# Kernel tuning notes

Hardware: AMD Instinct MI355X
Metric: run time of the kernel (lower is better)

Reference implementation:

```python
import jax, jax.numpy as jnp
import numpy as np

GAMMA = 2.0
EPS = 1e-6

B, C = 4096, 32000


def setup_inputs() -> dict:
    key = jax.random.key(0)
    k1, k2 = jax.random.split(key)
    pred = jax.random.normal(k1, (B, C), dtype=jnp.float32)
    target = jax.random.randint(k2, (B,), 0, C, dtype=jnp.int64)
    return {"pred": pred, "target": target}


def reference(pred, target):
    # pred: [B, C] logits, target: [B] int class labels
    b, c = pred.shape
    beta = (b - 1) / b
    logp = jax.nn.log_softmax(pred, axis=1)                      # [B, C]
    # Faithful to original: entropy_b = target_b * sum_c (1-p)^gamma * logp
    # (the torch code multiplies by the scalar class index b_target)
    focal = jnp.sum(jnp.power(1.0 - jnp.exp(logp), GAMMA) * logp, axis=1)  # [B]
    ent = target.astype(pred.dtype) * focal                     # [B]
    # class-balanced aggregation: bucket per class label
    counts = jax.ops.segment_sum(jnp.ones((b,), pred.dtype), target, num_segments=c)  # n_c
    cls_sum = jax.ops.segment_sum(ent, target, num_segments=c)  # sum of entropies per class
    w = (1.0 - beta) / (1.0 - jnp.power(jnp.asarray(beta, pred.dtype), counts) + EPS)
    # classes absent from batch have cls_sum == 0 exactly, so they contribute 0
    return (-1.0 / b) * jnp.sum(w * cls_sum)
```

## Files before the change

kernel.cpp:

```cpp
#include <hip/hip_runtime.h>
#include <math.h>

#define NROWS 4096
#define NCLS  32000
#define VEC_PER_ROW (NCLS / 4)
#define BLK 512
#define NV  16
#define TAIL (VEC_PER_ROW - (NV - 1) * BLK)
#define EPSF 1e-6f

#define LNBETA (-2.4417042724800387e-4f)
#define WNUM 2.44140625e-4f

__device__ __forceinline__ float max4(float4 v) {
    return fmaxf(fmaxf(v.x, v.y), fmaxf(v.z, v.w));
}
__device__ __forceinline__ float sum4(float4 v) {
    return (v.x + v.y) + (v.z + v.w);
}

__global__ __launch_bounds__(BLK, 4) void focal_kernel(const float* __restrict__ pred,
                                                       float* __restrict__ focal_out)
{
    const int row = blockIdx.x;
    const int tid = threadIdx.x;
    const float4* rp = reinterpret_cast<const float4*>(pred) + (size_t)row * VEC_PER_ROW;

    float4 x[NV];
#pragma unroll
    for (int i = 0; i < NV - 1; ++i) x[i] = rp[tid + i * BLK];
    const bool lv = tid < TAIL;
    if (lv) x[NV - 1] = rp[tid + (NV - 1) * BLK];
    else    x[NV - 1] = make_float4(-1e30f, -1e30f, -1e30f, -1e30f);

    float m = -1e30f, s1 = 0.0f;
#pragma unroll
    for (int i = 0; i < NV - 1; ++i) { m = fmaxf(m, max4(x[i])); s1 += sum4(x[i]); }
    m = fmaxf(m, max4(x[NV - 1]));
    if (lv) s1 += sum4(x[NV - 1]);

    __shared__ float sm[8], ss[8];
#pragma unroll
    for (int off = 32; off > 0; off >>= 1) {
        m  = fmaxf(m, __shfl_xor(m, off));
        s1 += __shfl_xor(s1, off);
    }
    const int wid  = tid >> 6;
    const int lane = tid & 63;
    if (lane == 0) { sm[wid] = m; ss[wid] = s1; }
    __syncthreads();
    if (tid < 64) {
        float mm = (tid < 8) ? sm[tid] : -1e30f;
        float s  = (tid < 8) ? ss[tid] : 0.0f;
#pragma unroll
        for (int off = 4; off > 0; off >>= 1) {
            mm = fmaxf(mm, __shfl_xor(mm, off));
            s += __shfl_xor(s, off);
        }
        if (tid == 0) { sm[0] = mm; ss[0] = s; }
    }
    __syncthreads();
    const float M  = sm[0];
    const float S1 = ss[0];

    float Z = 0.f, A = 0.f, Z2 = 0.f, A2 = 0.f;
#pragma unroll
    for (int i = 0; i < NV; ++i) {
        float vals[4] = {x[i].x, x[i].y, x[i].z, x[i].w};
#pragma unroll
        for (int j = 0; j < 4; ++j) {
            float t = vals[j] - M;
            float e = exp2f(t * 1.44269504088896340736f);
            Z += e;
            A = fmaf(e, t, A);
            float e2 = e * e;
            Z2 += e2;
            A2 = fmaf(e2, t, A2);
        }
    }

    __shared__ float r0[8], r1[8], r2[8], r3[8];
#pragma unroll
    for (int off = 32; off > 0; off >>= 1) {
        Z  += __shfl_xor(Z,  off);
        A  += __shfl_xor(A,  off);
        Z2 += __shfl_xor(Z2, off);
        A2 += __shfl_xor(A2, off);
    }
    if (lane == 0) { r0[wid] = Z; r1[wid] = A; r2[wid] = Z2; r3[wid] = A2; }
    __syncthreads();
    if (tid < 64) {
        float a = (tid < 8) ? r0[tid] : 0.f;
        float b = (tid < 8) ? r1[tid] : 0.f;
        float c = (tid < 8) ? r2[tid] : 0.f;
        float d = (tid < 8) ? r3[tid] : 0.f;
#pragma unroll
        for (int off = 4; off > 0; off >>= 1) {
            a += __shfl_xor(a, off);
            b += __shfl_xor(b, off);
            c += __shfl_xor(c, off);
            d += __shfl_xor(d, off);
        }
        if (tid == 0) {
            float lnZ  = log2f(a) * 0.69314718055994530942f;
            float invZ = 1.0f / a;
            float T = S1 - (float)NCLS * M;
            float focal = (T - (float)NCLS * lnZ)
                        - 2.0f * (b * invZ - lnZ)
                        + (d - lnZ * c) * (invZ * invZ);
            focal_out[row] = focal;
        }
    }
}

__global__ __launch_bounds__(1024) void finalize_kernel(const int* __restrict__ target,
                                                        const float* __restrict__ focal,
                                                        float* __restrict__ out)
{
    __shared__ unsigned int cnt[NCLS / 2];
    __shared__ double rd[16];
    const int tid = threadIdx.x;

    uint4* c4 = reinterpret_cast<uint4*>(cnt);
    for (int i = tid; i < NCLS / 8; i += 1024) c4[i] = make_uint4(0u, 0u, 0u, 0u);
    __syncthreads();

    for (int b = tid; b < NROWS; b += 1024) {
        int t = target[b];
        atomicAdd(&cnt[t >> 1], 1u << ((t & 1) * 16));
    }
    __syncthreads();

    double local = 0.0;
    for (int b = tid; b < NROWS; b += 1024) {
        int t = target[b];
        int n = (int)((cnt[t >> 1] >> ((t & 1) * 16)) & 0xffffu);
        float u = (float)n * LNBETA;
        float denom;
        if (u > -0.25f) {
            denom = -(u * (1.f + u * (0.5f + u * (0.16666667f + u * 0.041666667f))));
        } else {
            denom = 1.f - __expf(u);
        }
        float w = WNUM / (denom + EPSF);
        local += (double)(w * (float)t * focal[b]);
    }

#pragma unroll
    for (int off = 32; off > 0; off >>= 1) local += __shfl_xor(local, off);
    const int wid = tid >> 6, lane = tid & 63;
    if (lane == 0) rd[wid] = local;
    __syncthreads();
    if (tid < 64) {
        double v = (tid < 16) ? rd[tid] : 0.0;
#pragma unroll
        for (int off = 8; off > 0; off >>= 1) v += __shfl_xor(v, off);
        if (tid == 0) out[0] = (float)(v * (-1.0 / (double)NROWS));
    }
}

extern "C" void kernel_launch(void* const* d_in, const int* in_sizes, int n_in,
                              void* d_out, int out_size, void* d_ws, size_t ws_size,
                              hipStream_t stream)
{
    const float* pred  = (const float*)d_in[0];
    const int* target  = (const int*)d_in[1];
    float* out         = (float*)d_out;

    float* focal = (float*)d_ws;

    focal_kernel<<<NROWS, BLK, 0, stream>>>(pred, focal);
    finalize_kernel<<<1, 1024, 0, stream>>>(target, focal, out);
}
```

Before: 99.61 us.

## Fuse class-balanced finalize into focal kernel via per-row counts and atomics

Removes the single-block finalize kernel. Each row block now counts how many batch targets match its own label by scanning the whole target vector, computes its class weight, and atomically adds its weighted contribution to the output, which is zeroed with a memset first. This drops a serial one-block tail kernel and the focal workspace round trip. In exchange every block reads the full target array, 4096 float atomics hit one address, and the sum loses determinism and the double-precision accumulation.

```diff
diff --git a/kernel.cpp b/kernel.cpp
--- a/kernel.cpp
+++ b/kernel.cpp
@@ -8,6 +8,8 @@
 #define NV  16
 #define TAIL (VEC_PER_ROW - (NV - 1) * BLK)
 #define EPSF 1e-6f
+#define LN2  0.69314718055994530942f
+#define L2E  1.44269504088896340736f
 
 #define LNBETA (-2.4417042724800387e-4f)
 #define WNUM 2.44140625e-4f
@@ -20,7 +22,8 @@
 }
 
 __global__ __launch_bounds__(BLK, 4) void focal_kernel(const float* __restrict__ pred,
-                                                       float* __restrict__ focal_out)
+                                                       const int* __restrict__ target,
+                                                       float* __restrict__ out)
 {
     const int row = blockIdx.x;
     const int tid = threadIdx.x;
@@ -33,6 +36,13 @@
     if (lv) x[NV - 1] = rp[tid + (NV - 1) * BLK];
     else    x[NV - 1] = make_float4(-1e30f, -1e30f, -1e30f, -1e30f);
 
+    const int t_row = target[row];
+    const int4* tg = reinterpret_cast<const int4*>(target);
+    int4 ta = tg[tid];
+    int4 tb = tg[tid + BLK];
+    int cnt = (ta.x == t_row) + (ta.y == t_row) + (ta.z == t_row) + (ta.w == t_row)
+            + (tb.x == t_row) + (tb.y == t_row) + (tb.z == t_row) + (tb.w == t_row);
+
     float m = -1e30f, s1 = 0.0f;
 #pragma unroll
     for (int i = 0; i < NV - 1; ++i) { m = fmaxf(m, max4(x[i])); s1 += sum4(x[i]); }
@@ -40,24 +50,28 @@
     if (lv) s1 += sum4(x[NV - 1]);
 
     __shared__ float sm[8], ss[8];
+    __shared__ int   sc[8];
 #pragma unroll
     for (int off = 32; off > 0; off >>= 1) {
-        m  = fmaxf(m, __shfl_xor(m, off));
-        s1 += __shfl_xor(s1, off);
+        m   = fmaxf(m, __shfl_xor(m, off));
+        s1  += __shfl_xor(s1, off);
+        cnt += __shfl_xor(cnt, off);
     }
     const int wid  = tid >> 6;
     const int lane = tid & 63;
-    if (lane == 0) { sm[wid] = m; ss[wid] = s1; }
+    if (lane == 0) { sm[wid] = m; ss[wid] = s1; sc[wid] = cnt; }
     __syncthreads();
     if (tid < 64) {
         float mm = (tid < 8) ? sm[tid] : -1e30f;
         float s  = (tid < 8) ? ss[tid] : 0.0f;
+        int   cc = (tid < 8) ? sc[tid] : 0;
 #pragma unroll
         for (int off = 4; off > 0; off >>= 1) {
             mm = fmaxf(mm, __shfl_xor(mm, off));
             s += __shfl_xor(s, off);
+            cc += __shfl_xor(cc, off);
         }
-        if (tid == 0) { sm[0] = mm; ss[0] = s; }
+        if (tid == 0) { sm[0] = mm; ss[0] = s; sc[0] = cc; }
     }
     __syncthreads();
     const float M  = sm[0];
@@ -70,7 +84,7 @@
 #pragma unroll
         for (int j = 0; j < 4; ++j) {
             float t = vals[j] - M;
-            float e = exp2f(t * 1.44269504088896340736f);
+            float e = exp2f(t * L2E);
             Z += e;
             A = fmaf(e, t, A);
             float e2 = e * e;
@@ -102,60 +116,24 @@
             d += __shfl_xor(d, off);
         }
         if (tid == 0) {
-            float lnZ  = log2f(a) * 0.69314718055994530942f;
+            float lnZ  = log2f(a) * LN2;
             float invZ = 1.0f / a;
             float T = S1 - (float)NCLS * M;
             float focal = (T - (float)NCLS * lnZ)
                         - 2.0f * (b * invZ - lnZ)
                         + (d - lnZ * c) * (invZ * invZ);
-            focal_out[row] = focal;
+
+            int n = sc[0];
+            float u = (float)n * LNBETA;
+            float denom;
+            if (u > -0.25f) {
+                denom = -(u * (1.f + u * (0.5f + u * (0.16666667f + u * 0.041666667f))));
+            } else {
+                denom = 1.f - __expf(u);
+            }
+            float w = WNUM / (denom + EPSF);
+            atomicAdd(out, w * (float)t_row * focal * (-1.0f / (float)NROWS));
         }
-    }
-}
-
-__global__ __launch_bounds__(1024) void finalize_kernel(const int* __restrict__ target,
-                                                        const float* __restrict__ focal,
-                                                        float* __restrict__ out)
-{
-    __shared__ unsigned int cnt[NCLS / 2];
-    __shared__ double rd[16];
-    const int tid = threadIdx.x;
-
-    uint4* c4 = reinterpret_cast<uint4*>(cnt);
-    for (int i = tid; i < NCLS / 8; i += 1024) c4[i] = make_uint4(0u, 0u, 0u, 0u);
-    __syncthreads();
-
-    for (int b = tid; b < NROWS; b += 1024) {
-        int t = target[b];
-        atomicAdd(&cnt[t >> 1], 1u << ((t & 1) * 16));
-    }
-    __syncthreads();
-
-    double local = 0.0;
-    for (int b = tid; b < NROWS; b += 1024) {
-        int t = target[b];
-        int n = (int)((cnt[t >> 1] >> ((t & 1) * 16)) & 0xffffu);
-        float u = (float)n * LNBETA;
-        float denom;
-        if (u > -0.25f) {
-            denom = -(u * (1.f + u * (0.5f + u * (0.16666667f + u * 0.041666667f))));
-        } else {
-            denom = 1.f - __expf(u);
-        }
-        float w = WNUM / (denom + EPSF);
-        local += (double)(w * (float)t * focal[b]);
-    }
-
-#pragma unroll
-    for (int off = 32; off > 0; off >>= 1) local += __shfl_xor(local, off);
-    const int wid = tid >> 6, lane = tid & 63;
-    if (lane == 0) rd[wid] = local;
-    __syncthreads();
-    if (tid < 64) {
-        double v = (tid < 16) ? rd[tid] : 0.0;
-#pragma unroll
-        for (int off = 8; off > 0; off >>= 1) v += __shfl_xor(v, off);
-        if (tid == 0) out[0] = (float)(v * (-1.0 / (double)NROWS));
     }
 }
 
@@ -167,8 +145,6 @@
     const int* target  = (const int*)d_in[1];
     float* out         = (float*)d_out;
 
-    float* focal = (float*)d_ws;
-
-    focal_kernel<<<NROWS, BLK, 0, stream>>>(pred, focal);
-    finalize_kernel<<<1, 1024, 0, stream>>>(target, focal, out);
+    hipMemsetAsync(out, 0, sizeof(float), stream);
+    focal_kernel<<<NROWS, BLK, 0, stream>>>(pred, target, out);
 }
```

Measured after the change: 104.2 us. 4.6% more time.
